# Kernel optimization log

Hardware: AMD Instinct MI355X
Metric: run time of the kernel (lower is better)

Reference implementation:

```python
import jax, jax.numpy as jnp
from jax import lax
import numpy as np


def conv(x, w, b):
    # x: [N,C,H,W], w: [O,I,kh,kw] (torch layout), VALID padding, stride 1
    y = lax.conv_general_dilated(x, w, (1, 1), 'VALID',
                                 dimension_numbers=('NCHW', 'OIHW', 'NCHW'))
    return y + b[None, :, None, None]


def prelu4(x, a):
    return jnp.where(x > 0, x, a[None, :, None, None] * x)


def prelu1(x, a):
    return jnp.where(x > 0, x, a * x)


def maxpool_ceil(x, k, s):
    # torch MaxPool2d(k, s, ceil_mode=True): pad right/bottom so last partial window counts
    def pad_amt(n):
        out = -(-(n - k) // s) + 1  # ceil((n-k)/s)+1
        return max((out - 1) * s + k - n, 0)
    ph, pw = pad_amt(x.shape[2]), pad_amt(x.shape[3])
    return lax.reduce_window(x, -jnp.inf, lax.max, (1, 1, k, k), (1, 1, s, s),
                             [(0, 0), (0, 0), (0, ph), (0, pw)])


def setup_inputs() -> dict:
    key = jax.random.key(0)
    ks = iter(jax.random.split(key, 64))
    def rn(shape, s=0.05):
        return jax.random.normal(next(ks), shape, dtype=jnp.float32) * s
    p = {}
    p['imgs'] = rn((8, 3, 720, 720), 1.0)
    p['crops24'] = rn((2048, 3, 24, 24), 1.0)
    p['crops48'] = rn((512, 3, 48, 48), 1.0)
    # PNet
    p['pw1'] = rn((10, 3, 3, 3)); p['pb1'] = rn((10,)); p['pa1'] = jnp.full((10,), 0.25, jnp.float32)
    p['pw2'] = rn((16, 10, 3, 3)); p['pb2'] = rn((16,)); p['pa2'] = jnp.full((16,), 0.25, jnp.float32)
    p['pw3'] = rn((32, 16, 3, 3)); p['pb3'] = rn((32,)); p['pa3'] = jnp.full((32,), 0.25, jnp.float32)
    p['pw41'] = rn((2, 32, 1, 1)); p['pb41'] = rn((2,))
    p['pw42'] = rn((4, 32, 1, 1)); p['pb42'] = rn((4,))
    # RNet
    p['rw1'] = rn((28, 3, 3, 3)); p['rb1'] = rn((28,)); p['ra1'] = jnp.full((28,), 0.25, jnp.float32)
    p['rw2'] = rn((48, 28, 3, 3)); p['rb2'] = rn((48,)); p['ra2'] = jnp.full((48,), 0.25, jnp.float32)
    p['rw3'] = rn((64, 48, 2, 2)); p['rb3'] = rn((64,)); p['ra3'] = jnp.full((64,), 0.25, jnp.float32)
    p['rd4w'] = rn((128, 576)); p['rd4b'] = rn((128,)); p['ra4'] = jnp.full((128,), 0.25, jnp.float32)
    p['rd51w'] = rn((2, 128)); p['rd51b'] = rn((2,))
    p['rd52w'] = rn((4, 128)); p['rd52b'] = rn((4,))
    # ONet
    p['ow1'] = rn((32, 3, 3, 3)); p['ob1'] = rn((32,)); p['oa1'] = jnp.full((32,), 0.25, jnp.float32)
    p['ow2'] = rn((64, 32, 3, 3)); p['ob2'] = rn((64,)); p['oa2'] = jnp.full((64,), 0.25, jnp.float32)
    p['ow3'] = rn((64, 64, 3, 3)); p['ob3'] = rn((64,)); p['oa3'] = jnp.full((64,), 0.25, jnp.float32)
    p['ow4'] = rn((128, 64, 2, 2)); p['ob4'] = rn((128,)); p['oa4'] = jnp.full((128,), 0.25, jnp.float32)
    p['od5w'] = rn((256, 1152)); p['od5b'] = rn((256,)); p['oa5'] = jnp.full((256,), 0.25, jnp.float32)
    p['od61w'] = rn((2, 256)); p['od61b'] = rn((2,))
    p['od62w'] = rn((4, 256)); p['od62b'] = rn((4,))
    p['od63w'] = rn((10, 256)); p['od63b'] = rn((10,))
    return p


def reference(imgs, crops24, crops48,
              pw1, pb1, pa1, pw2, pb2, pa2, pw3, pb3, pa3, pw41, pb41, pw42, pb42,
              rw1, rb1, ra1, rw2, rb2, ra2, rw3, rb3, ra3, rd4w, rd4b, ra4,
              rd51w, rd51b, rd52w, rd52b,
              ow1, ob1, oa1, ow2, ob2, oa2, ow3, ob3, oa3, ow4, ob4, oa4,
              od5w, od5b, oa5, od61w, od61b, od62w, od62b, od63w, od63b):
    # --- PNet (fully convolutional, stage 1) ---
    x = prelu4(conv(imgs, pw1, pb1), pa1)
    x = maxpool_ceil(x, 2, 2)
    x = prelu4(conv(x, pw2, pb2), pa2)
    x = prelu4(conv(x, pw3, pb3), pa3)
    p_prob = jax.nn.softmax(conv(x, pw41, pb41), axis=1)  # [B,2,Hp,Wp]
    p_reg = conv(x, pw42, pb42)                            # [B,4,Hp,Wp]
    # --- RNet (24x24 crops, stage 2) ---
    x = prelu4(conv(crops24, rw1, rb1), ra1)
    x = maxpool_ceil(x, 3, 2)
    x = prelu4(conv(x, rw2, rb2), ra2)
    x = maxpool_ceil(x, 3, 2)
    x = prelu4(conv(x, rw3, rb3), ra3)
    x = jnp.transpose(x, (0, 3, 2, 1)).reshape(x.shape[0], -1)  # permute(0,3,2,1).view
    x = prelu1(x @ rd4w.T + rd4b, ra4)
    r_a = jax.nn.softmax(x @ rd51w.T + rd51b, axis=1)  # [N,2]
    r_b = x @ rd52w.T + rd52b                           # [N,4]
    # --- ONet (48x48 crops, stage 3) ---
    x = prelu4(conv(crops48, ow1, ob1), oa1)
    x = maxpool_ceil(x, 3, 2)
    x = prelu4(conv(x, ow2, ob2), oa2)
    x = maxpool_ceil(x, 3, 2)
    x = prelu4(conv(x, ow3, ob3), oa3)
    x = maxpool_ceil(x, 2, 2)
    x = prelu4(conv(x, ow4, ob4), oa4)
    x = jnp.transpose(x, (0, 3, 2, 1)).reshape(x.shape[0], -1)
    x = prelu1(x @ od5w.T + od5b, oa5)
    o_a = jax.nn.softmax(x @ od61w.T + od61b, axis=1)  # [M,2]
    o_b = x @ od62w.T + od62b                           # [M,4]
    o_c = x @ od63w.T + od63b                           # [M,10]
    return (p_reg, p_prob, r_b, r_a, o_b, o_c, o_a)
```

## Files before the change

kernel.cpp:

```cpp
#include <hip/hip_runtime.h>
#include <hip/hip_bf16.h>

typedef __hip_bfloat16 bf16;
typedef unsigned short u16;
typedef unsigned int u32;

typedef float f32x16 __attribute__((ext_vector_type(16)));
typedef short s16x8 __attribute__((ext_vector_type(8)));

__device__ __forceinline__ float b2f(bf16 v) { return __bfloat162float(v); }
__device__ __forceinline__ bf16  f2b(float v) { return __float2bfloat16(v); }
__device__ __forceinline__ float us2f(u16 u) { return __uint_as_float((u32)u << 16); }
__device__ __forceinline__ float ulo(u32 u)  { return __uint_as_float(u << 16); }
__device__ __forceinline__ float uhi(u32 u)  { return __uint_as_float(u & 0xFFFF0000u); }

#define OFF_IMGS 0
#define OFF_C24  12441600
#define OFF_C48  15980544
#define OFF_WTS  19519488
#define OFF_A    20119488
#define OFF_B    54819488
#define OFF_RW   71319488
#define RW_RC2   (OFF_RW)
#define RW_RC3   (OFF_RW + 18432)
#define RW_OC2   (OFF_RW + 30720)
#define RW_OC3   (OFF_RW + 49152)
#define RW_OC4   (OFF_RW + 86016)
#define RW_PC1   (OFF_RW + 118784)
#define RW_PC2   (OFF_RW + 123392)
#define RW_PC3   (OFF_RW + 128000)
#define ARENA_N  (OFF_RW + 132608L)

__device__ bf16 g_arena[ARENA_N];
__device__ int  g_isf32;

__global__ void detect_kern(const void* imgs)
{
    if (threadIdx.x != 0) return;
    const u16* u = (const u16*)imgs;
    int f32 = 0;
    for (int i = 0; i < 256; ++i) {
        int e = (u[i] >> 7) & 0xFF;
        if (e >= 0x8D) f32 = 1;
    }
    g_isf32 = f32;
}

__global__ void convert_kern(const void* __restrict__ src, int dst_off, int n)
{
    int i = blockIdx.x * blockDim.x + threadIdx.x;
    if (i >= n) return;
    float v = g_isf32 ? ((const float*)src)[i] : b2f(((const bf16*)src)[i]);
    g_arena[(long)dst_off + i] = f2b(v);
}

__global__ void convert_img_kern(const void* __restrict__ src, int dst_off, int n)
{
    int i = blockIdx.x * blockDim.x + threadIdx.x;
    if (i >= n) return;
    int c = i % 3;
    int t = i / 3;
    int x = t % 720;
    int t2 = t / 720;
    int y = t2 % 720;
    int nn = t2 / 720;
    long si = ((long)(nn * 3 + c) * 720 + y) * 720 + x;
    float v = g_isf32 ? ((const float*)src)[si] : b2f(((const bf16*)src)[si]);
    g_arena[(long)dst_off + i] = f2b(v);
}

struct CvtEnt { const void* src; int dst_off; int n; };
struct CvtTab { CvtEnt e[50]; };
__global__ void convert_many_kern(CvtTab tab)
{
    CvtEnt ent = tab.e[blockIdx.y];
    int i = blockIdx.x * blockDim.x + threadIdx.x;
    if (i >= ent.n) return;
    float v = g_isf32 ? ((const float*)ent.src)[i] : b2f(((const bf16*)ent.src)[i]);
    g_arena[(long)ent.dst_off + i] = f2b(v);
}

__device__ __forceinline__ void stout(void* base, long idx, float v, int f32)
{
    if (f32) ((float*)base)[idx] = v;
    else     ((bf16*)base)[idx] = f2b(v);
}

__global__ void repack_w_kern(int w_off, int rw_off, int CO, int CIN, int CPAD,
                              int KHW, int total)
{
    int i = blockIdx.x * blockDim.x + threadIdx.x;
    if (i >= total) return;
    int c = i % CPAD;
    int t = i / CPAD;
    int g = t % KHW;
    int o = t / KHW;
    u16 v = 0;
    if (o < CO && c < CIN)
        v = ((const u16*)g_arena)[w_off + ((long)(o * CIN + c)) * KHW + g];
    ((u16*)g_arena)[(long)rw_off + i] = v;
}

template<int CIN,int KH,int KW,int H,int W,int OH,int OW,int CO,int OBLK,int R>
__launch_bounds__(256)
__global__ void conv_a_kern(int in_off, int w_off, int b_off, int a_off, int out_off)
{
    constexpr int KTOT = CIN * KH * KW;
    constexpr int INCNT = CIN * H * W;
    constexpr int OPT = OBLK / 8;
    constexpr int NPX = OH * OW;
    constexpr int PBLK = 32 * R;
    __shared__ __align__(16) u16 in_s[INCNT];
    __shared__ __align__(16) u16 w_s[KTOT * OBLK];
    __shared__ __align__(16) u16 out_s[PBLK * CO];

    int n = blockIdx.x, pxc = blockIdx.y;
    const u16* ga = (const u16*)g_arena;

    const u32* src = (const u32*)(ga + in_off + (long)n * INCNT);
    u32* dst = (u32*)in_s;
    for (int i = threadIdx.x; i < INCNT / 2; i += 256) dst[i] = src[i];
    for (int i = threadIdx.x; i < KTOT * OBLK; i += 256) {
        int o_l = i % OBLK, k = i / OBLK;
        w_s[i] = (o_l < CO) ? ga[w_off + (long)o_l * KTOT + k] : (u16)0;
    }
    __syncthreads();

    int lane = threadIdx.x & 31, og = threadIdx.x >> 5;
    int pixoff[R];
    bool vld[R];
    #pragma unroll
    for (int r = 0; r < R; ++r) {
        int px = pxc * PBLK + lane + r * 32;
        vld[r] = px < NPX;
        int p = vld[r] ? px : 0;
        pixoff[r] = (p / OW) * W + (p % OW);
    }
    float acc[R][OPT];
    #pragma unroll
    for (int r = 0; r < R; ++r)
        #pragma unroll
        for (int j = 0; j < OPT; ++j) acc[r][j] = 0.f;

    const u32* wu = (const u32*)w_s;
    for (int c = 0; c < CIN; ++c) {
        #pragma unroll
        for (int ky = 0; ky < KH; ++ky) {
            #pragma unroll
            for (int kx = 0; kx < KW; ++kx) {
                int k = (c * KH + ky) * KW + kx;
                int ub = c * (H * W) + ky * W + kx;
                float a[R];
                #pragma unroll
                for (int r = 0; r < R; ++r) a[r] = us2f(in_s[ub + pixoff[r]]);
                int wb = (k * OBLK + og * OPT) >> 1;
                float wv[OPT];
                #pragma unroll
                for (int jj = 0; jj < OPT / 2; ++jj) {
                    u32 u = wu[wb + jj];
                    wv[2 * jj] = ulo(u); wv[2 * jj + 1] = uhi(u);
                }
                #pragma unroll
                for (int r = 0; r < R; ++r)
                    #pragma unroll
                    for (int j = 0; j < OPT; ++j)
                        acc[r][j] += a[r] * wv[j];
            }
        }
    }
    #pragma unroll
    for (int j = 0; j < OPT; ++j) {
        int o = og * OPT + j;
        if (o < CO) {
            float b = us2f(ga[b_off + o]);
            float al = us2f(ga[a_off + o]);
            #pragma unroll
            for (int r = 0; r < R; ++r) if (vld[r]) {
                float v = acc[r][j] + b;
                v = v > 0.f ? v : v * al;
                u16 bits; bf16 t = f2b(v); __builtin_memcpy(&bits, &t, 2);
                out_s[(lane + r * 32) * CO + o] = bits;
            }
        }
    }
    __syncthreads();
    int base_px = pxc * PBLK;
    int npx_blk = NPX - base_px; if (npx_blk > PBLK) npx_blk = PBLK;
    int tot8 = (npx_blk * CO) >> 3;
    uint4* gout = (uint4*)&g_arena[(long)out_off + ((long)n * NPX + base_px) * CO];
    const uint4* osrc = (const uint4*)out_s;
    for (int i = threadIdx.x; i < tot8; i += 256) gout[i] = osrc[i];
}

template<int CIN,int CPAD,int KH,int KW,int H,int W,int OH,int OW,int CO,int NT>
__launch_bounds__(256, 2)
__global__ void conv_mfma_kern(int in_off, int rw_off, int b_off, int a_off, int out_off)
{
    constexpr int NPX = OH * OW;
    constexpr int MT = (NPX + 31) / 32;
    constexpr int PST = CPAD + 8;
    constexpr int NCH = CPAD / 16;
    constexpr int KHW = KH * KW;
    constexpr int NG = KHW * NCH;
    __shared__ __align__(16) u16 patchT[H * W * PST];

    int n = blockIdx.x;
    const u16* ga = (const u16*)g_arena;
    const u16* in = ga + in_off + (long)n * (H * W * CIN);

    if constexpr (CIN == CPAD) {
        constexpr int NV = H * W * (CPAD / 8);
        for (int i = threadIdx.x; i < NV; i += 256) {
            int pix = i / (CPAD / 8), j = i % (CPAD / 8);
            *(s16x8*)&patchT[pix * PST + j * 8] = *(const s16x8*)&in[pix * CPAD + j * 8];
        }
    } else {
        constexpr int TOT = H * W * CPAD;
        for (int i = threadIdx.x; i < TOT; i += 256) {
            int pix = i / CPAD, c = i % CPAD;
            patchT[pix * PST + c] = (c < CIN) ? in[pix * CIN + c] : (u16)0;
        }
    }
    __syncthreads();

    int m = threadIdx.x & 31, half = (threadIdx.x >> 5) & 1, wave = threadIdx.x >> 6;
    int c0 = half * 8;
    int nt = wave % NT;
    int o = nt * 32 + m;
    bool ovld = o < CO;
    float bb = ovld ? us2f(ga[b_off + o]) : 0.f;
    float aa = ovld ? us2f(ga[a_off + o]) : 0.f;

    s16x8 bfrag[NG];
    const u16* wb = ga + rw_off + (long)(nt * 32 + m) * (KHW * CPAD) + c0;
    #pragma unroll
    for (int g = 0; g < NG; ++g)
        bfrag[g] = *(const s16x8*)(wb + g * 16);

    for (int mt = wave / NT; mt < MT; mt += 4 / NT) {
        int p = mt * 32 + m;
        int pc = p < NPX ? p : NPX - 1;
        int pp = (pc / OW) * W + (pc % OW);
        f32x16 acc = {};
        #pragma unroll
        for (int t = 0; t < KHW; ++t) {
            int rb = (pp + (t / KW) * W + (t % KW)) * PST + c0;
            #pragma unroll
            for (int ch = 0; ch < NCH; ++ch) {
                s16x8 a = *(const s16x8*)&patchT[rb + ch * 16];
                acc = __builtin_amdgcn_mfma_f32_32x32x16_bf16(a, bfrag[t * NCH + ch], acc, 0, 0, 0);
            }
        }
        if (ovld) {
            bf16* op = g_arena + (long)out_off + (long)n * (NPX * CO) + o;
            #pragma unroll
            for (int reg = 0; reg < 16; ++reg) {
                int mrow = (reg & 3) + 8 * (reg >> 2) + 4 * half;
                int pr = mt * 32 + mrow;
                if (pr < NPX) {
                    float v = acc[reg] + bb;
                    v = v > 0.f ? v : v * aa;
                    op[(long)pr * CO] = f2b(v);
                }
            }
        }
    }
}

__launch_bounds__(256)
__global__ void pnet_c1m_kern(int b_off, int a_off, int out_off)
{
    constexpr int PST = 24;
    __shared__ __align__(16) u16 patchT[612 * PST];
    __shared__ __align__(16) u16 out_s[8 * 16 * 10];
    __shared__ float b1s[16], a1s[16];

    int n = blockIdx.x, by = blockIdx.y, tx = blockIdx.z;
    int gy0 = by * 16, gx0 = tx * 32;
    const u16* ga = (const u16*)g_arena;

    for (int i = threadIdx.x; i < 1224; i += 256) {
        int pix = i >> 1, slot = i & 1;
        *(s16x8*)&patchT[pix * PST + slot * 8] = (s16x8){};
    }
    if (threadIdx.x < 16) {
        b1s[threadIdx.x] = (threadIdx.x < 10) ? us2f(ga[b_off + threadIdx.x]) : 0.f;
        a1s[threadIdx.x] = (threadIdx.x < 10) ? us2f(ga[a_off + threadIdx.x]) : 0.f;
    }
    __syncthreads();

    for (int i = threadIdx.x; i < 18 * 128; i += 256) {
        int py = i >> 7, r = i & 127;
        if (r < 102) {
            int pxx = r / 3, c = r - pxx * 3;
            int iy = gy0 + py, ix = gx0 + pxx;
            if (iy < 720 && ix < 720)
                patchT[(py * 34 + pxx) * PST + c] =
                    ga[OFF_IMGS + (((long)n * 720 + iy) * 720 + ix) * 3 + c];
        }
    }
    __syncthreads();

    int lane = threadIdx.x & 63, w = threadIdx.x >> 6;
    int half = lane >> 5, m = lane & 31;
    int c0 = half * 8;

    s16x8 bfrag[9];
    {
        const u16* wbp = ga + RW_PC1 + m * 144 + c0;
        #pragma unroll
        for (int g = 0; g < 9; ++g)
            bfrag[g] = *(const s16x8*)(wbp + g * 16);
    }

    f32x16 acc[4] = {};
    #pragma unroll
    for (int g = 0; g < 9; ++g) {
        int ky = g / 3, kx = g % 3;
        #pragma unroll
        for (int rj = 0; rj < 4; ++rj) {
            s16x8 a = *(const s16x8*)&patchT[((4 * w + rj + ky) * 34 + m + kx) * PST + c0];
            acc[rj] = __builtin_amdgcn_mfma_f32_32x32x16_bf16(a, bfrag[g], acc[rj], 0, 0, 0);
        }
    }

    if (m < 10) {
        float b = b1s[m], al = a1s[m];
        #pragma unroll
        for (int s = 0; s < 2; ++s) {
            int lr = 2 * w + s;
            #pragma unroll
            for (int u = 0; u < 8; ++u) {
                int pxo = (u & 1) + 4 * (u >> 1) + 2 * half;
                float v0 = acc[2 * s][2 * u] + b;         v0 = v0 > 0.f ? v0 : v0 * al;
                float v1 = acc[2 * s][2 * u + 1] + b;     v1 = v1 > 0.f ? v1 : v1 * al;
                float v2 = acc[2 * s + 1][2 * u] + b;     v2 = v2 > 0.f ? v2 : v2 * al;
                float v3 = acc[2 * s + 1][2 * u + 1] + b; v3 = v3 > 0.f ? v3 : v3 * al;
                float mx = fmaxf(fmaxf(v0, v1), fmaxf(v2, v3));
                u16 bits; bf16 t = f2b(mx); __builtin_memcpy(&bits, &t, 2);
                out_s[(lr * 16 + pxo) * 10 + m] = bits;
            }
        }
    }
    __syncthreads();

    int nrowv = 359 - by * 8; if (nrowv > 8) nrowv = 8;
    int ncolv = 359 - tx * 16; if (ncolv > 16) ncolv = 16;
    int cw = ncolv * 5;
    int totw = nrowv * cw;
    for (int i = threadIdx.x; i < totw; i += 256) {
        int j = i / cw, rem = i - j * cw;
        u32 v = ((const u32*)out_s)[j * 80 + rem];
        *(u32*)&g_arena[(long)out_off +
            (((long)n * 359 + by * 8 + j) * 359 + tx * 16) * 10 + rem * 2] = v;
    }
}

__launch_bounds__(256)
__global__ void pnet_c2m_kern(int in_off, int b_off, int a_off, int out_off)
{
    constexpr int PST = 24;
    __shared__ __align__(16) u16 patchT[340 * PST];
    __shared__ float b2s[16], a2s[16];

    int n = blockIdx.x, by = blockIdx.y, tx = blockIdx.z;
    int gy0 = by * 8, gx0 = tx * 32;
    const u16* ga = (const u16*)g_arena;

    for (int i = threadIdx.x; i < 5440; i += 256) {
        int pix = i >> 4, c = i & 15;
        int py = pix / 34, pxx = pix % 34;
        int iy = gy0 + py, ix = gx0 + pxx;
        u16 v = 0;
        if (c < 10 && iy < 359 && ix < 359)
            v = ga[in_off + ((long)(n * 359 + iy) * 359 + ix) * 10 + c];
        patchT[pix * PST + c] = v;
    }
    if (threadIdx.x < 16) {
        b2s[threadIdx.x] = us2f(ga[b_off + threadIdx.x]);
        a2s[threadIdx.x] = us2f(ga[a_off + threadIdx.x]);
    }
    __syncthreads();

    int lane = threadIdx.x & 63, w = threadIdx.x >> 6;
    int half = lane >> 5, m = lane & 31;
    int c0 = half * 8;

    s16x8 bfrag[9];
    {
        const u16* wbp = ga + RW_PC2 + m * 144 + c0;
        #pragma unroll
        for (int g = 0; g < 9; ++g)
            bfrag[g] = *(const s16x8*)(wbp + g * 16);
    }

    f32x16 acc0 = {}, acc1 = {};
    #pragma unroll
    for (int g = 0; g < 9; ++g) {
        int ky = g / 3, kx = g % 3;
        s16x8 a0 = *(const s16x8*)&patchT[((2 * w + 0 + ky) * 34 + m + kx) * PST + c0];
        s16x8 a1 = *(const s16x8*)&patchT[((2 * w + 1 + ky) * 34 + m + kx) * PST + c0];
        acc0 = __builtin_amdgcn_mfma_f32_32x32x16_bf16(a0, bfrag[g], acc0, 0, 0, 0);
        acc1 = __builtin_amdgcn_mfma_f32_32x32x16_bf16(a1, bfrag[g], acc1, 0, 0, 0);
    }

    if (m < 16) {
        float b = b2s[m], al = a2s[m];
        #pragma unroll
        for (int reg = 0; reg < 16; ++reg) {
            int mrow = (reg & 3) + 8 * (reg >> 2) + 4 * half;
            int gy = gy0 + 2 * w, gx = gx0 + mrow;
            if (gy < 357 && gx < 357) {
                float v = acc0[reg] + b; v = v > 0.f ? v : v * al;
                g_arena[(long)out_off + (((long)(n * 357 + gy)) * 357 + gx) * 16 + m] = f2b(v);
            }
            if (gy + 1 < 357 && gx < 357) {
                float v = acc1[reg] + b; v = v > 0.f ? v : v * al;
                g_arena[(long)out_off + (((long)(n * 357 + gy + 1)) * 357 + gx) * 16 + m] = f2b(v);
            }
        }
    }
}

__launch_bounds__(256)
__global__ void pnet_c3h_kern(int in_off, int b3o, int a3o,
                              int w41o, int b41o, int w42o, int b42o, void* dout)
{
    constexpr int PST = 24;
    __shared__ __align__(16) u16 patchT[340 * PST];
    __shared__ float c3s[256 * 33];
    __shared__ float b3f[32], a3f[32], w41f[64], w42f[128], b41f[2], b42f[4];

    int n = blockIdx.x, by = blockIdx.y, tx = blockIdx.z;
    int gy0 = by * 8, gx0 = tx * 32;
    const u16* ga = (const u16*)g_arena;

    for (int i = threadIdx.x; i < 680; i += 256) {
        int pix = i >> 1, h = i & 1;
        int py = pix / 34, pxx = pix % 34;
        int iy = gy0 + py, ix = gx0 + pxx;
        s16x8 v = {};
        if (iy < 357 && ix < 357)
            v = *(const s16x8*)&ga[in_off + (((long)(n * 357 + iy)) * 357 + ix) * 16 + h * 8];
        *(s16x8*)&patchT[pix * PST + h * 8] = v;
    }
    for (int i = threadIdx.x; i < 32; i += 256) { b3f[i] = us2f(ga[b3o + i]); a3f[i] = us2f(ga[a3o + i]); }
    for (int i = threadIdx.x; i < 64; i += 256) w41f[i] = us2f(ga[w41o + i]);
    for (int i = threadIdx.x; i < 128; i += 256) w42f[i] = us2f(ga[w42o + i]);
    if (threadIdx.x < 2) b41f[threadIdx.x] = us2f(ga[b41o + threadIdx.x]);
    if (threadIdx.x < 4) b42f[threadIdx.x] = us2f(ga[b42o + threadIdx.x]);
    __syncthreads();

    int lane = threadIdx.x & 63, w = threadIdx.x >> 6;
    int half = lane >> 5, m = lane & 31;
    int c0 = half * 8;

    s16x8 bfrag[9];
    {
        const u16* wbp = ga + RW_PC3 + m * 144 + c0;
        #pragma unroll
        for (int g = 0; g < 9; ++g)
            bfrag[g] = *(const s16x8*)(wbp + g * 16);
    }

    f32x16 acc0 = {}, acc1 = {};
    #pragma unroll
    for (int g = 0; g < 9; ++g) {
        int ky = g / 3, kx = g % 3;
        s16x8 a0 = *(const s16x8*)&patchT[((2 * w + 0 + ky) * 34 + m + kx) * PST + c0];
        s16x8 a1 = *(const s16x8*)&patchT[((2 * w + 1 + ky) * 34 + m + kx) * PST + c0];
        acc0 = __builtin_amdgcn_mfma_f32_32x32x16_bf16(a0, bfrag[g], acc0, 0, 0, 0);
        acc1 = __builtin_amdgcn_mfma_f32_32x32x16_bf16(a1, bfrag[g], acc1, 0, 0, 0);
    }

    {
        float b = b3f[m], al = a3f[m];
        #pragma unroll
        for (int reg = 0; reg < 16; ++reg) {
            int mrow = (reg & 3) + 8 * (reg >> 2) + 4 * half;
            float v0 = acc0[reg] + b; v0 = v0 > 0.f ? v0 : v0 * al;
            c3s[(w * 64 + mrow) * 33 + m] = v0;
            float v1 = acc1[reg] + b; v1 = v1 > 0.f ? v1 : v1 * al;
            c3s[(w * 64 + 32 + mrow) * 33 + m] = v1;
        }
    }
    __syncthreads();

    int p = threadIdx.x;
    int gy = gy0 + (p >> 5), gx = gx0 + (p & 31);
    if (gy < 355 && gx < 355) {
        int f32 = g_isf32;
        float l0 = b41f[0], l1 = b41f[1];
        float r0 = b42f[0], r1 = b42f[1], r2 = b42f[2], r3 = b42f[3];
        #pragma unroll
        for (int o = 0; o < 32; ++o) {
            float v = c3s[p * 33 + o];
            l0 += v * w41f[o];
            l1 += v * w41f[32 + o];
            r0 += v * w42f[o];
            r1 += v * w42f[32 + o];
            r2 += v * w42f[64 + o];
            r3 += v * w42f[96 + o];
        }
        float mx = fmaxf(l0, l1);
        float e0 = __expf(l0 - mx), e1 = __expf(l1 - mx);
        float inv = 1.f / (e0 + e1);
        const long HW = 355L * 355L;
        long pix = (long)gy * 355 + gx;
        stout(dout, 4032800 + ((long)n * 2 + 0) * HW + pix, e0 * inv, f32);
        stout(dout, 4032800 + ((long)n * 2 + 1) * HW + pix, e1 * inv, f32);
        stout(dout, ((long)n * 4 + 0) * HW + pix, r0, f32);
        stout(dout, ((long)n * 4 + 1) * HW + pix, r1, f32);
        stout(dout, ((long)n * 4 + 2) * HW + pix, r2, f32);
        stout(dout, ((long)n * 4 + 3) * HW + pix, r3, f32);
    }
}

__global__ void maxpool_nhwc_kern(int in_off, int out_off, int C, int H, int W,
                                  int OH, int OW, int k, int s, int total)
{
    int tid = blockIdx.x * blockDim.x + threadIdx.x;
    if (tid >= total) return;
    int c = tid % C; int t = tid / C;
    int ox = t % OW; t /= OW;
    int oy = t % OH; int n = t / OH;
    const u16* ip = (const u16*)g_arena + in_off + (long)n * H * W * C + c;
    int sy = oy * s, sx = ox * s;
    float m = -1e30f;
    for (int ky = 0; ky < k; ++ky) {
        int iy = sy + ky;
        if (iy >= H) break;
        for (int kx = 0; kx < k; ++kx) {
            int ix = sx + kx;
            if (ix >= W) break;
            m = fmaxf(m, us2f(ip[(iy * W + ix) * C]));
        }
    }
    g_arena[(long)out_off + tid] = f2b(m);
}

__global__ void flatten_hw_kern(int in_off, int out_off, int C, int H, int W, int total)
{
    int tid = blockIdx.x * blockDim.x + threadIdx.x;
    if (tid >= total) return;
    int CHW = C * H * W;
    int n = tid / CHW;
    int k = tid % CHW;
    int w = k / (H * C);
    int r = k % (H * C);
    int h = r / C;
    int c = r % C;
    g_arena[(long)out_off + tid] =
        g_arena[(long)in_off + ((long)n * H * W + h * W + w) * C + c];
}

__launch_bounds__(256)
__global__ void dense_tile_kern(int in_off, int w_off, int b_off, int a_off, int out_off,
                                int K, int J)
{
    __shared__ u16 in_s[32 * 66];
    __shared__ u16 w_s[32 * 66];
    int n0 = blockIdx.x * 32, j0 = blockIdx.y * 32;
    const u16* ga = (const u16*)g_arena;
    const u16* fin = ga + in_off;
    const u16* wts = ga + w_off;
    int sy = threadIdx.x >> 4, sx = threadIdx.x & 15;

    float acc00 = 0.f, acc01 = 0.f, acc10 = 0.f, acc11 = 0.f;

    for (int kc = 0; kc < K; kc += 64) {
        #pragma unroll
        for (int it = 0; it < 4; ++it) {
            int i = threadIdx.x + it * 256;
            int row = i >> 5, c2 = i & 31;
            u32 v = *(const u32*)(fin + (long)(n0 + row) * K + kc + c2 * 2);
            *(u32*)&in_s[row * 66 + c2 * 2] = v;
            u32 wv = *(const u32*)(wts + (long)(j0 + row) * K + kc + c2 * 2);
            *(u32*)&w_s[row * 66 + c2 * 2] = wv;
        }
        __syncthreads();
        #pragma unroll
        for (int kk = 0; kk < 64; ++kk) {
            float a0 = us2f(in_s[(2 * sy) * 66 + kk]);
            float a1 = us2f(in_s[(2 * sy + 1) * 66 + kk]);
            float b0 = us2f(w_s[(2 * sx) * 66 + kk]);
            float b1 = us2f(w_s[(2 * sx + 1) * 66 + kk]);
            acc00 += a0 * b0; acc01 += a0 * b1;
            acc10 += a1 * b0; acc11 += a1 * b1;
        }
        __syncthreads();
    }

    float accs[2][2] = {{acc00, acc01}, {acc10, acc11}};
    #pragma unroll
    for (int jj = 0; jj < 2; ++jj) {
        int j = j0 + 2 * sx + jj;
        float b = us2f(ga[b_off + j]);
        float al = us2f(ga[a_off + j]);
        #pragma unroll
        for (int ss = 0; ss < 2; ++ss) {
            int n = n0 + 2 * sy + ss;
            float v = accs[ss][jj] + b;
            v = v > 0.f ? v : v * al;
            g_arena[(long)out_off + (long)n * J + j] = f2b(v);
        }
    }
}

template<int K, int J1, int J2>
__launch_bounds__(256)
__global__ void heads_wave_kern(int fc_off, int wSo, int bSo, int w1o, int b1o,
                                int w2o, int b2o, void* dout,
                                long outS_off, long out1_off, long out2_off, int N)
{
    constexpr int KPL = K / 64;
    constexpr int NACC = 2 + J1 + J2;
    int wave = (blockIdx.x * blockDim.x + threadIdx.x) >> 6;
    int lane = threadIdx.x & 63;
    if (wave >= N) return;
    const u16* ga = (const u16*)g_arena;
    const u16* f  = ga + fc_off + (long)wave * K;
    const u16* wS = ga + wSo;
    const u16* w1 = ga + w1o;
    const u16* w2 = ga + w2o;

    float acc[NACC];
    #pragma unroll
    for (int j = 0; j < NACC; ++j) acc[j] = 0.f;

    #pragma unroll
    for (int kk = 0; kk < KPL; ++kk) {
        int k = lane + kk * 64;
        float fv = us2f(f[k]);
        acc[0] += fv * us2f(wS[k]);
        acc[1] += fv * us2f(wS[K + k]);
        #pragma unroll
        for (int j = 0; j < J1; ++j)
            acc[2 + j] += fv * us2f(w1[j * K + k]);
        #pragma unroll
        for (int j = 0; j < J2; ++j)
            acc[2 + J1 + j] += fv * us2f(w2[j * K + k]);
    }
    #pragma unroll
    for (int j = 0; j < NACC; ++j)
        #pragma unroll
        for (int off = 32; off > 0; off >>= 1)
            acc[j] += __shfl_xor(acc[j], off, 64);

    if (lane == 0) {
        int f32 = g_isf32;
        float l0 = acc[0] + us2f(ga[bSo + 0]);
        float l1 = acc[1] + us2f(ga[bSo + 1]);
        float m = fmaxf(l0, l1);
        float e0 = __expf(l0 - m), e1 = __expf(l1 - m);
        float inv = 1.f / (e0 + e1);
        stout(dout, outS_off + (long)wave * 2 + 0, e0 * inv, f32);
        stout(dout, outS_off + (long)wave * 2 + 1, e1 * inv, f32);
        #pragma unroll
        for (int j = 0; j < J1; ++j)
            stout(dout, out1_off + (long)wave * J1 + j, acc[2 + j] + us2f(ga[b1o + j]), f32);
        #pragma unroll
        for (int j = 0; j < J2; ++j)
            stout(dout, out2_off + (long)wave * J2 + j, acc[2 + J1 + j] + us2f(ga[b2o + j]), f32);
    }
}

static inline dim3 g1(int total) { return dim3((unsigned)((total + 255) / 256)); }

extern "C" void kernel_launch(void* const* d_in, const int* in_sizes, int n_in,
                              void* d_out, int out_size, void* d_ws, size_t ws_size,
                              hipStream_t stream)
{
    int woff[53];
    int acc = OFF_WTS;
    int mx = 0;
    for (int i = 3; i < 53; ++i) { woff[i] = acc; acc += in_sizes[i]; if (in_sizes[i] > mx) mx = in_sizes[i]; }

    detect_kern<<<1, 64, 0, stream>>>(d_in[0]);
    convert_img_kern<<<g1(12441600), 256, 0, stream>>>(d_in[0], OFF_IMGS, 12441600);
    convert_kern<<<g1(3538944), 256, 0, stream>>>(d_in[1], OFF_C24, 3538944);
    convert_kern<<<g1(3538944), 256, 0, stream>>>(d_in[2], OFF_C48, 3538944);
    CvtTab tab;
    for (int i = 3; i < 53; ++i) tab.e[i - 3] = CvtEnt{ d_in[i], woff[i], in_sizes[i] };
    convert_many_kern<<<dim3((unsigned)((mx + 255) / 256), 50), 256, 0, stream>>>(tab);

    repack_w_kern<<<g1(4608), 256, 0, stream>>>(woff[3], RW_PC1, 10, 3, 16, 9, 4608);
    repack_w_kern<<<g1(4608), 256, 0, stream>>>(woff[6], RW_PC2, 16, 10, 16, 9, 4608);
    repack_w_kern<<<g1(4608), 256, 0, stream>>>(woff[9], RW_PC3, 32, 16, 16, 9, 4608);
    repack_w_kern<<<g1(18432), 256, 0, stream>>>(woff[19], RW_RC2, 48, 28, 32, 9, 18432);
    repack_w_kern<<<g1(12288), 256, 0, stream>>>(woff[22], RW_RC3, 64, 48, 48, 4, 12288);
    repack_w_kern<<<g1(18432), 256, 0, stream>>>(woff[35], RW_OC2, 64, 32, 32, 9, 18432);
    repack_w_kern<<<g1(36864), 256, 0, stream>>>(woff[38], RW_OC3, 64, 64, 64, 9, 36864);
    repack_w_kern<<<g1(32768), 256, 0, stream>>>(woff[41], RW_OC4, 128, 64, 64, 4, 32768);

    pnet_c1m_kern<<<dim3(8, 45, 23), 256, 0, stream>>>(woff[4], woff[5], OFF_A);
    pnet_c2m_kern<<<dim3(8, 45, 12), 256, 0, stream>>>(OFF_A, woff[7], woff[8], OFF_B);
    pnet_c3h_kern<<<dim3(8, 45, 12), 256, 0, stream>>>(OFF_B,
        woff[10], woff[11], woff[12], woff[13], woff[14], woff[15], d_out);

    conv_a_kern<3,3,3,24,24,22,22,28,32,4><<<dim3(2048, 4, 1), 256, 0, stream>>>(
        OFF_C24, woff[16], woff[17], woff[18], OFF_A);
    maxpool_nhwc_kern<<<g1(6938624), 256, 0, stream>>>(OFF_A, OFF_B, 28, 22, 22, 11, 11, 3, 2, 6938624);
    conv_mfma_kern<28,32,3,3,11,11,9,9,48,2><<<dim3(2048), 256, 0, stream>>>(
        OFF_B, RW_RC2, woff[20], woff[21], OFF_A);
    maxpool_nhwc_kern<<<g1(1572864), 256, 0, stream>>>(OFF_A, OFF_B, 48, 9, 9, 4, 4, 3, 2, 1572864);
    conv_mfma_kern<48,48,2,2,4,4,3,3,64,2><<<dim3(2048), 256, 0, stream>>>(
        OFF_B, RW_RC3, woff[23], woff[24], OFF_A);
    flatten_hw_kern<<<g1(1179648), 256, 0, stream>>>(OFF_A, OFF_B, 64, 3, 3, 1179648);
    dense_tile_kern<<<dim3(64, 4), 256, 0, stream>>>(OFF_B, woff[25], woff[26], woff[27], OFF_A,
        576, 128);
    heads_wave_kern<128,4,0><<<dim3(512), 256, 0, stream>>>(OFF_A,
        woff[28], woff[29], woff[30], woff[31], 0, 0,
        d_out, 6057392L, 6049200L, 0L, 2048);

    conv_a_kern<3,3,3,48,48,46,46,32,32,4><<<dim3(512, 17, 1), 256, 0, stream>>>(
        OFF_C48, woff[32], woff[33], woff[34], OFF_A);
    maxpool_nhwc_kern<<<g1(8667136), 256, 0, stream>>>(OFF_A, OFF_B, 32, 46, 46, 23, 23, 3, 2, 8667136);
    conv_mfma_kern<32,32,3,3,23,23,21,21,64,2><<<dim3(512), 256, 0, stream>>>(
        OFF_B, RW_OC2, woff[36], woff[37], OFF_A);
    maxpool_nhwc_kern<<<g1(3276800), 256, 0, stream>>>(OFF_A, OFF_B, 64, 21, 21, 10, 10, 3, 2, 3276800);
    conv_mfma_kern<64,64,3,3,10,10,8,8,64,2><<<dim3(512), 256, 0, stream>>>(
        OFF_B, RW_OC3, woff[39], woff[40], OFF_A);
    maxpool_nhwc_kern<<<g1(524288), 256, 0, stream>>>(OFF_A, OFF_B, 64, 8, 8, 4, 4, 2, 2, 524288);
    conv_mfma_kern<64,64,2,2,4,4,3,3,128,4><<<dim3(512), 256, 0, stream>>>(
        OFF_B, RW_OC4, woff[42], woff[43], OFF_A);
    flatten_hw_kern<<<g1(589824), 256, 0, stream>>>(OFF_A, OFF_B, 128, 3, 3, 589824);
    dense_tile_kern<<<dim3(16, 8), 256, 0, stream>>>(OFF_B, woff[44], woff[45], woff[46], OFF_A,
        1152, 256);
    heads_wave_kern<256,4,10><<<dim3(128), 256, 0, stream>>>(OFF_A,
        woff[47], woff[48], woff[49], woff[50], woff[51], woff[52],
        d_out, 6068656L, 6061488L, 6063536L, 512);
}
```

Baseline: 924.2 us.

## Replace scalar first-layer RNet/ONet convs with MFMA kernels on NHWC crops

Measured after the change: 858.3 us. 7.1% less time.

```diff
diff --git a/kernel.cpp b/kernel.cpp
--- a/kernel.cpp
+++ b/kernel.cpp
@@ -29,7 +29,9 @@
 #define RW_PC1   (OFF_RW + 118784)
 #define RW_PC2   (OFF_RW + 123392)
 #define RW_PC3   (OFF_RW + 128000)
-#define ARENA_N  (OFF_RW + 132608L)
+#define RW_RC1   (OFF_RW + 132608)
+#define RW_OC1   (OFF_RW + 137216)
+#define ARENA_N  (OFF_RW + 141824L)
 
 __device__ bf16 g_arena[ARENA_N];
 __device__ int  g_isf32;
@@ -44,14 +46,6 @@
         if (e >= 0x8D) f32 = 1;
     }
     g_isf32 = f32;
-}
-
-__global__ void convert_kern(const void* __restrict__ src, int dst_off, int n)
-{
-    int i = blockIdx.x * blockDim.x + threadIdx.x;
-    if (i >= n) return;
-    float v = g_isf32 ? ((const float*)src)[i] : b2f(((const bf16*)src)[i]);
-    g_arena[(long)dst_off + i] = f2b(v);
 }
 
 __global__ void convert_img_kern(const void* __restrict__ src, int dst_off, int n)
@@ -69,6 +63,19 @@
     g_arena[(long)dst_off + i] = f2b(v);
 }
 
+__global__ void convert_crop_kern(const void* __restrict__ src, int dst_off, int HW, int n)
+{
+    int i = blockIdx.x * blockDim.x + threadIdx.x;
+    if (i >= n) return;
+    int c = i % 3;
+    int t = i / 3;
+    int pix = t % HW;
+    int nn = t / HW;
+    long si = ((long)(nn * 3 + c)) * HW + pix;
+    float v = g_isf32 ? ((const float*)src)[si] : b2f(((const bf16*)src)[si]);
+    g_arena[(long)dst_off + i] = f2b(v);
+}
+
 struct CvtEnt { const void* src; int dst_off; int n; };
 struct CvtTab { CvtEnt e[50]; };
 __global__ void convert_many_kern(CvtTab tab)
@@ -101,95 +108,85 @@
     ((u16*)g_arena)[(long)rw_off + i] = v;
 }
 
-template<int CIN,int KH,int KW,int H,int W,int OH,int OW,int CO,int OBLK,int R>
+template<int H,int W,int OH,int OW,int CO>
 __launch_bounds__(256)
-__global__ void conv_a_kern(int in_off, int w_off, int b_off, int a_off, int out_off)
-{
-    constexpr int KTOT = CIN * KH * KW;
-    constexpr int INCNT = CIN * H * W;
-    constexpr int OPT = OBLK / 8;
-    constexpr int NPX = OH * OW;
-    constexpr int PBLK = 32 * R;
-    __shared__ __align__(16) u16 in_s[INCNT];
-    __shared__ __align__(16) u16 w_s[KTOT * OBLK];
-    __shared__ __align__(16) u16 out_s[PBLK * CO];
-
-    int n = blockIdx.x, pxc = blockIdx.y;
+__global__ void conv1_mfma_kern(int in_off, int rw_off, int b_off, int a_off, int out_off)
+{
+    constexpr int PST = 8;
+    constexpr int CO2 = CO + 2;
+    __shared__ __align__(16) u16 patchT[10 * W * PST];
+    __shared__ __align__(16) u16 out_s[8 * 32 * CO2];
+
+    int n = blockIdx.x, by = blockIdx.y, tx = blockIdx.z;
+    int gy0 = by * 8, gx0 = tx * 32;
     const u16* ga = (const u16*)g_arena;
 
-    const u32* src = (const u32*)(ga + in_off + (long)n * INCNT);
-    u32* dst = (u32*)in_s;
-    for (int i = threadIdx.x; i < INCNT / 2; i += 256) dst[i] = src[i];
-    for (int i = threadIdx.x; i < KTOT * OBLK; i += 256) {
-        int o_l = i % OBLK, k = i / OBLK;
-        w_s[i] = (o_l < CO) ? ga[w_off + (long)o_l * KTOT + k] : (u16)0;
-    }
-    __syncthreads();
-
-    int lane = threadIdx.x & 31, og = threadIdx.x >> 5;
-    int pixoff[R];
-    bool vld[R];
-    #pragma unroll
-    for (int r = 0; r < R; ++r) {
-        int px = pxc * PBLK + lane + r * 32;
-        vld[r] = px < NPX;
-        int p = vld[r] ? px : 0;
-        pixoff[r] = (p / OW) * W + (p % OW);
-    }
-    float acc[R][OPT];
-    #pragma unroll
-    for (int r = 0; r < R; ++r)
-        #pragma unroll
-        for (int j = 0; j < OPT; ++j) acc[r][j] = 0.f;
-
-    const u32* wu = (const u32*)w_s;
-    for (int c = 0; c < CIN; ++c) {
-        #pragma unroll
-        for (int ky = 0; ky < KH; ++ky) {
+    for (int i = threadIdx.x; i < 10 * W; i += 256)
+        *(s16x8*)&patchT[i * PST] = (s16x8){};
+    __syncthreads();
+    for (int i = threadIdx.x; i < 10 * W * 3; i += 256) {
+        int py = i / (W * 3), r = i - py * (W * 3);
+        if (gy0 + py < H)
+            patchT[(py * W + r / 3) * PST + r % 3] =
+                ga[in_off + ((long)(n * H + gy0 + py) * W) * 3 + r];
+    }
+    __syncthreads();
+
+    int lane = threadIdx.x & 63, w = threadIdx.x >> 6;
+    int half = lane >> 5, m = lane & 31;
+    int c0 = half * 8;
+
+    s16x8 bfrag[9];
+    {
+        const u16* wbp = ga + rw_off + m * 144 + c0;
+        #pragma unroll
+        for (int g = 0; g < 9; ++g)
+            bfrag[g] = *(const s16x8*)(wbp + g * 16);
+    }
+    float bb = (m < CO) ? us2f(ga[b_off + m]) : 0.f;
+    float aa = (m < CO) ? us2f(ga[a_off + m]) : 0.f;
+
+    s16x8 azero = {};
+    f32x16 acc0 = {}, acc1 = {};
+    #pragma unroll
+    for (int g = 0; g < 9; ++g) {
+        int ky = g / 3, kx = g % 3;
+        int cx = gx0 + m + kx; if (cx > W - 1) cx = W - 1;
+        s16x8 a0 = half ? azero : *(const s16x8*)&patchT[((2 * w + 0 + ky) * W + cx) * PST];
+        s16x8 a1 = half ? azero : *(const s16x8*)&patchT[((2 * w + 1 + ky) * W + cx) * PST];
+        acc0 = __builtin_amdgcn_mfma_f32_32x32x16_bf16(a0, bfrag[g], acc0, 0, 0, 0);
+        acc1 = __builtin_amdgcn_mfma_f32_32x32x16_bf16(a1, bfrag[g], acc1, 0, 0, 0);
+    }
+
+    if (m < CO) {
+        #pragma unroll
+        for (int s = 0; s < 2; ++s) {
+            const f32x16& A = s ? acc1 : acc0;
+            int r = 2 * w + s;
             #pragma unroll
-            for (int kx = 0; kx < KW; ++kx) {
-                int k = (c * KH + ky) * KW + kx;
-                int ub = c * (H * W) + ky * W + kx;
-                float a[R];
-                #pragma unroll
-                for (int r = 0; r < R; ++r) a[r] = us2f(in_s[ub + pixoff[r]]);
-                int wb = (k * OBLK + og * OPT) >> 1;
-                float wv[OPT];
-                #pragma unroll
-                for (int jj = 0; jj < OPT / 2; ++jj) {
-                    u32 u = wu[wb + jj];
-                    wv[2 * jj] = ulo(u); wv[2 * jj + 1] = uhi(u);
-                }
-                #pragma unroll
-                for (int r = 0; r < R; ++r)
-                    #pragma unroll
-                    for (int j = 0; j < OPT; ++j)
-                        acc[r][j] += a[r] * wv[j];
+            for (int reg = 0; reg < 16; ++reg) {
+                int x = (reg & 3) + 8 * (reg >> 2) + 4 * half;
+                float v = A[reg] + bb;
+                v = v > 0.f ? v : v * aa;
+                u16 bits; bf16 t = f2b(v); __builtin_memcpy(&bits, &t, 2);
+                out_s[(r * 32 + x) * CO2 + m] = bits;
             }
         }
     }
-    #pragma unroll
-    for (int j = 0; j < OPT; ++j) {
-        int o = og * OPT + j;
-        if (o < CO) {
-            float b = us2f(ga[b_off + o]);
-            float al = us2f(ga[a_off + o]);
-            #pragma unroll
-            for (int r = 0; r < R; ++r) if (vld[r]) {
-                float v = acc[r][j] + b;
-                v = v > 0.f ? v : v * al;
-                u16 bits; bf16 t = f2b(v); __builtin_memcpy(&bits, &t, 2);
-                out_s[(lane + r * 32) * CO + o] = bits;
-            }
-        }
-    }
-    __syncthreads();
-    int base_px = pxc * PBLK;
-    int npx_blk = NPX - base_px; if (npx_blk > PBLK) npx_blk = PBLK;
-    int tot8 = (npx_blk * CO) >> 3;
-    uint4* gout = (uint4*)&g_arena[(long)out_off + ((long)n * NPX + base_px) * CO];
-    const uint4* osrc = (const uint4*)out_s;
-    for (int i = threadIdx.x; i < tot8; i += 256) gout[i] = osrc[i];
+    __syncthreads();
+
+    int nrowv = OH - gy0; if (nrowv > 8) nrowv = 8;
+    int ncolv = OW - gx0; if (ncolv > 32) ncolv = 32;
+    int cw = ncolv * (CO / 2);
+    int totw = nrowv * cw;
+    const u32* osrc = (const u32*)out_s;
+    for (int i = threadIdx.x; i < totw; i += 256) {
+        int r = i / cw, rem = i - r * cw;
+        int x = rem / (CO / 2), op = rem - x * (CO / 2);
+        u32 v = osrc[(r * 32 + x) * (CO2 / 2) + op];
+        *(u32*)&g_arena[(long)out_off +
+            (((long)(n * OH + gy0 + r)) * OW + gx0 + x) * CO + 2 * op] = v;
+    }
 }
 
 template<int CIN,int CPAD,int KH,int KW,int H,int W,int OH,int OW,int CO,int NT>
@@ -678,8 +675,8 @@
 
     detect_kern<<<1, 64, 0, stream>>>(d_in[0]);
     convert_img_kern<<<g1(12441600), 256, 0, stream>>>(d_in[0], OFF_IMGS, 12441600);
-    convert_kern<<<g1(3538944), 256, 0, stream>>>(d_in[1], OFF_C24, 3538944);
-    convert_kern<<<g1(3538944), 256, 0, stream>>>(d_in[2], OFF_C48, 3538944);
+    convert_crop_kern<<<g1(3538944), 256, 0, stream>>>(d_in[1], OFF_C24, 576, 3538944);
+    convert_crop_kern<<<g1(3538944), 256, 0, stream>>>(d_in[2], OFF_C48, 2304, 3538944);
     CvtTab tab;
     for (int i = 3; i < 53; ++i) tab.e[i - 3] = CvtEnt{ d_in[i], woff[i], in_sizes[i] };
     convert_many_kern<<<dim3((unsigned)((mx + 255) / 256), 50), 256, 0, stream>>>(tab);
@@ -687,8 +684,10 @@
     repack_w_kern<<<g1(4608), 256, 0, stream>>>(woff[3], RW_PC1, 10, 3, 16, 9, 4608);
     repack_w_kern<<<g1(4608), 256, 0, stream>>>(woff[6], RW_PC2, 16, 10, 16, 9, 4608);
     repack_w_kern<<<g1(4608), 256, 0, stream>>>(woff[9], RW_PC3, 32, 16, 16, 9, 4608);
+    repack_w_kern<<<g1(4608), 256, 0, stream>>>(woff[16], RW_RC1, 28, 3, 16, 9, 4608);
     repack_w_kern<<<g1(18432), 256, 0, stream>>>(woff[19], RW_RC2, 48, 28, 32, 9, 18432);
     repack_w_kern<<<g1(12288), 256, 0, stream>>>(woff[22], RW_RC3, 64, 48, 48, 4, 12288);
+    repack_w_kern<<<g1(4608), 256, 0, stream>>>(woff[32], RW_OC1, 32, 3, 16, 9, 4608);
     repack_w_kern<<<g1(18432), 256, 0, stream>>>(woff[35], RW_OC2, 64, 32, 32, 9, 18432);
     repack_w_kern<<<g1(36864), 256, 0, stream>>>(woff[38], RW_OC3, 64, 64, 64, 9, 36864);
     repack_w_kern<<<g1(32768), 256, 0, stream>>>(woff[41], RW_OC4, 128, 64, 64, 4, 32768);
@@ -698,8 +697,8 @@
     pnet_c3h_kern<<<dim3(8, 45, 12), 256, 0, stream>>>(OFF_B,
         woff[10], woff[11], woff[12], woff[13], woff[14], woff[15], d_out);
 
-    conv_a_kern<3,3,3,24,24,22,22,28,32,4><<<dim3(2048, 4, 1), 256, 0, stream>>>(
-        OFF_C24, woff[16], woff[17], woff[18], OFF_A);
+    conv1_mfma_kern<24,24,22,22,28><<<dim3(2048, 3, 1), 256, 0, stream>>>(
+        OFF_C24, RW_RC1, woff[17], woff[18], OFF_A);
     maxpool_nhwc_kern<<<g1(6938624), 256, 0, stream>>>(OFF_A, OFF_B, 28, 22, 22, 11, 11, 3, 2, 6938624);
     conv_mfma_kern<28,32,3,3,11,11,9,9,48,2><<<dim3(2048), 256, 0, stream>>>(
         OFF_B, RW_RC2, woff[20], woff[21], OFF_A);
@@ -713,8 +712,8 @@
         woff[28], woff[29], woff[30], woff[31], 0, 0,
         d_out, 6057392L, 6049200L, 0L, 2048);
 
-    conv_a_kern<3,3,3,48,48,46,46,32,32,4><<<dim3(512, 17, 1), 256, 0, stream>>>(
-        OFF_C48, woff[32], woff[33], woff[34], OFF_A);
+    conv1_mfma_kern<48,48,46,46,32><<<dim3(512, 6, 2), 256, 0, stream>>>(
+        OFF_C48, RW_OC1, woff[33], woff[34], OFF_A);
     maxpool_nhwc_kern<<<g1(8667136), 256, 0, stream>>>(OFF_A, OFF_B, 32, 46, 46, 23, 23, 3, 2, 8667136);
     conv_mfma_kern<32,32,3,3,23,23,21,21,64,2><<<dim3(512), 256, 0, stream>>>(
         OFF_B, RW_OC2, woff[36], woff[37], OFF_A);
```
